# Kernel tuning notes

Hardware: AMD Instinct MI355X
Metric: run time of the kernel (lower is better)

## Reference

```python
import jax, jax.numpy as jnp
import numpy as np


def gcn_conv(x, edge_index, W, b):
    """PyG-style GCNConv: add self loops, symmetric normalization, sum-aggregate."""
    N = x.shape[0]
    loop = jnp.arange(N, dtype=edge_index.dtype)
    src = jnp.concatenate([edge_index[0], loop])
    dst = jnp.concatenate([edge_index[1], loop])
    # degree computed on target (col) index with unit edge weights
    deg = jax.ops.segment_sum(jnp.ones_like(dst, dtype=x.dtype), dst, num_segments=N)
    dinv = jnp.where(deg > 0, jax.lax.rsqrt(deg), 0.0)
    norm = dinv[src] * dinv[dst]            # [E+N]
    h = x @ W                               # [N, out]
    msg = h[src] * norm[:, None]            # gather + scale
    out = jax.ops.segment_sum(msg, dst, num_segments=N)  # scatter-add
    return out + b


def global_mean_pool(x, batch, num_graphs):
    s = jax.ops.segment_sum(x, batch, num_segments=num_graphs)
    cnt = jax.ops.segment_sum(jnp.ones((x.shape[0],), x.dtype), batch, num_segments=num_graphs)
    return s / jnp.maximum(cnt, 1.0)[:, None]


NUM_GRAPHS = 64


def setup_inputs() -> dict:
    key = jax.random.key(0)
    ks = jax.random.split(key, 20)
    N, E = 100000, 1600000
    inp = {
        "x_origin": jax.random.normal(ks[0], (N, 25), jnp.float32),
        "edge_index_origin": jax.random.randint(ks[1], (2, E), 0, N, jnp.int64),
        "batch_origin": jnp.sort(jax.random.randint(ks[2], (N,), 0, NUM_GRAPHS, jnp.int64)),
        "x_line": jax.random.normal(ks[3], (N, 51), jnp.float32),
        "edge_index_line": jax.random.randint(ks[4], (2, E), 0, N, jnp.int64),
        "batch_line": jnp.sort(jax.random.randint(ks[5], (N,), 0, NUM_GRAPHS, jnp.int64)),
        # learned params (Glorot-ish scale)
        "W1": jax.random.normal(ks[6], (25, 128), jnp.float32) * 0.1,
        "b1": jnp.zeros((128,), jnp.float32),
        "W2": jax.random.normal(ks[7], (128, 64), jnp.float32) * 0.08,
        "b2": jnp.zeros((64,), jnp.float32),
        "W5": jax.random.normal(ks[8], (64, 5), jnp.float32) * 0.1,
        "b5": jnp.zeros((5,), jnp.float32),
        "W3": jax.random.normal(ks[9], (51, 64), jnp.float32) * 0.1,
        "b3": jnp.zeros((64,), jnp.float32),
        "W4": jax.random.normal(ks[10], (64, 5), jnp.float32) * 0.1,
        "b4": jnp.zeros((5,), jnp.float32),
        "Wfc": jax.random.normal(ks[11], (10, 2), jnp.float32) * 0.2,
        "bfc": jnp.zeros((2,), jnp.float32),
    }
    return inp


def reference(x_origin, edge_index_origin, batch_origin,
              x_line, edge_index_line, batch_line,
              W1, b1, W2, b2, W5, b5, W3, b3, W4, b4, Wfc, bfc):
    # origin branch
    h = jax.nn.relu(gcn_conv(x_origin, edge_index_origin, W1, b1))
    h = jax.nn.relu(gcn_conv(h, edge_index_origin, W2, b2))
    h = gcn_conv(h, edge_index_origin, W5, b5)
    g_origin = global_mean_pool(h, batch_origin, NUM_GRAPHS)  # [G, 5]
    # line branch
    hl = jax.nn.relu(gcn_conv(x_line, edge_index_line, W3, b3))
    hl = gcn_conv(hl, edge_index_line, W4, b4)
    g_line = global_mean_pool(hl, batch_line, NUM_GRAPHS)     # [G, 5]
    x = jnp.concatenate([g_origin, g_line], axis=1) @ Wfc + bfc  # [G, 2]
    return jax.nn.log_softmax(x, axis=1)
```

## Files before the change

### kernel.cpp

```cpp
#include <hip/hip_runtime.h>
#include <math.h>

#define NUM_G 64
#define CAP 32
#define SL 128
#define CHUNK_Q 1024
#define SEGCAP 32
#define MAXR 800
#define MAXNBA 1024
#define LSTR 33
#define ABLK 512

typedef unsigned short u16;
typedef unsigned int u32;
typedef int vint4 __attribute__((ext_vector_type(4)));
typedef short bf16x8 __attribute__((ext_vector_type(8)));
typedef float f32x4 __attribute__((ext_vector_type(4)));

__device__ inline u16 f2bf(float f) {
    u32 u = __float_as_uint(f);
    u32 r = u + 0x7FFF + ((u >> 16) & 1);
    return (u16)(r >> 16);
}
__device__ inline float bf2f(u16 h) { return __uint_as_float((u32)h << 16); }
__device__ inline float bflo(u32 p) { return __uint_as_float(p << 16); }
__device__ inline float bfhi(u32 p) { return __uint_as_float(p & 0xFFFF0000u); }

__device__ inline int slice_of(int d, float pinv) {
    int s = (int)((float)d * pinv);
    return s > SL - 1 ? SL - 1 : s;
}


__global__ void k_bin(const int* __restrict__ ei_o, const int* __restrict__ ei_l,
                      u32* __restrict__ binbuf, int* __restrict__ cntbuf,
                      int E, int NBA, float pinv) {
    __shared__ int lcnt[2 * SL];
    for (int i = threadIdx.x; i < 2 * SL; i += 256) lcnt[i] = 0;
    __syncthreads();
    const int qE = E >> 2;
    const int TQ = 2 * qE;
    const int b = blockIdx.x;
    for (int k = 0; k < CHUNK_Q; k += 256) {
        int qi = b * CHUNK_Q + k + threadIdx.x;
        if (qi >= TQ) break;
        int g = qi >= qE;
        int e4 = (g ? qi - qE : qi) * 4;
        const int* ei = g ? ei_l : ei_o;
        vint4 d4 = __builtin_nontemporal_load((const vint4*)(ei + E + e4));
        vint4 s4 = __builtin_nontemporal_load((const vint4*)(ei + e4));
        #pragma unroll
        for (int j = 0; j < 4; j++) {
            int d = d4[j];
            int bin = g * SL + slice_of(d, pinv);
            int rank = atomicAdd(&lcnt[bin], 1);
            if (rank < SEGCAP) {
                u32 pk = ((u32)(d & 1023) << 17) | (u32)s4[j];
                binbuf[((size_t)(bin * NBA + b)) * SEGCAP + rank] = pk;
            }
        }
    }
    __syncthreads();
    for (int i = threadIdx.x; i < 2 * SL; i += 256)
        cntbuf[i * NBA + b] = min(lcnt[i], SEGCAP);
}

__global__ __launch_bounds__(ABLK, 1)
void k_assemble(const u32* __restrict__ binbuf, const int* __restrict__ cntbuf,
                const int* __restrict__ ei_o, const int* __restrict__ ei_l,
                int* __restrict__ adj_o, int* __restrict__ adj_l,
                int* __restrict__ deg_o, int* __restrict__ deg_l,
                float* __restrict__ dinv_o, float* __restrict__ dinv_l,
                const float* __restrict__ x_o, const float* __restrict__ x_l,
                u16* __restrict__ Xpo, u16* __restrict__ Xpl,
                int N, int E, int NBA, float pinv) {
    const int g = blockIdx.x >> 7;
    const int s = blockIdx.x & (SL - 1);

    int lo, hi;
    { int a = 0, b2 = N; while (a < b2) { int m = (a + b2) >> 1;
        if (slice_of(m, pinv) >= s) b2 = m; else a = m + 1; } lo = a; }
    { int a = lo, b2 = N; while (a < b2) { int m = (a + b2) >> 1;
        if (slice_of(m, pinv) >= s + 1) b2 = m; else a = m + 1; } hi = a; }
    const int R = hi - lo;

    __shared__ int ladj[MAXR * LSTR];
    __shared__ int cnt[MAXR];
    __shared__ int segcnt[MAXNBA];
    __shared__ float sdinv[MAXR];
    for (int i = threadIdx.x; i < R; i += ABLK) cnt[i] = 0;
    const int bin = g * SL + s;
    for (int i = threadIdx.x; i < NBA; i += ABLK) segcnt[i] = cntbuf[bin * NBA + i];
    __syncthreads();

    const u32* base = binbuf + (size_t)bin * NBA * SEGCAP;
    const int total = NBA * SEGCAP;
    const int lo10 = lo & 1023;
    for (int i = threadIdx.x; i < total; i += ABLK) {
        int seg = i >> 5;
        int idx = i & (SEGCAP - 1);
        if (idx >= segcnt[seg]) continue;
        u32 pk = __builtin_nontemporal_load(base + i);
        int drel = ((int)(pk >> 17) - lo10) & 1023;
        int src = (int)(pk & 0x1FFFFu);
        int r = atomicAdd(&cnt[drel], 1);
        if (r < CAP) ladj[drel * LSTR + r] = src;
    }
    int tbase = (E >> 2) * 4, rem = E - tbase;
    if (threadIdx.x < rem) {
        const int* ei = g ? ei_l : ei_o;
        int e = tbase + threadIdx.x;
        int d = ei[E + e];
        if (d >= lo && d < hi) {
            int r = atomicAdd(&cnt[d - lo], 1);
            if (r < CAP) ladj[(d - lo) * LSTR + r] = ei[e];
        }
    }
    __syncthreads();

    for (int r = threadIdx.x; r < R; r += ABLK) {
        int c = min(cnt[r], CAP);
        int* row = &ladj[r * LSTR];
        int v[CAP];
        #pragma unroll
        for (int a = 0; a < CAP; a++) v[a] = (a < c) ? row[a] : 0x7FFFFFFF;
        #pragma unroll
        for (int k = 2; k <= CAP; k <<= 1) {
            #pragma unroll
            for (int j = k >> 1; j > 0; j >>= 1) {
                #pragma unroll
                for (int i = 0; i < CAP; i++) {
                    int ixj = i ^ j;
                    if (ixj > i) {
                        bool up = ((i & k) == 0);
                        int a = v[i], b = v[ixj];
                        bool sw = up ? (a > b) : (a < b);
                        v[i] = sw ? b : a;
                        v[ixj] = sw ? a : b;
                    }
                }
            }
        }
        #pragma unroll
        for (int a = 0; a < CAP; a++) row[a] = v[a];
    }
    __syncthreads();

    int* adj = g ? adj_l : adj_o;
    int* deg = g ? deg_l : deg_o;
    float* dinv = g ? dinv_l : dinv_o;
    for (int i = threadIdx.x; i < R * CAP; i += ABLK) {
        int r = i >> 5, c = i & 31;
        adj[(size_t)lo * CAP + i] = ladj[r * LSTR + c];
    }
    for (int i = threadIdx.x; i < R; i += ABLK) {
        int c = cnt[i];
        deg[lo + i] = c;
        float dv = rsqrtf((float)(c + 1));
        dinv[lo + i] = dv;
        sdinv[i] = dv;
    }
    __syncthreads();

    const float* xsrc = g ? x_l : x_o;
    u16* Xp = g ? Xpl : Xpo;
    const int FR = g ? 51 : 25;
    const int SH = g ? 6 : 5;
    const int FC = 1 << SH;
    for (int i = threadIdx.x; i < (R << SH); i += ABLK) {
        int r = i >> SH, c = i & (FC - 1);
        float val = (c < FR) ? xsrc[(size_t)(lo + r) * FR + c] * sdinv[r] : 0.f;
        Xp[((size_t)(lo + r) << SH) + c] = f2bf(val);
    }
}


template <int K, int F, int MODE>
__device__ void gemm_body(u16* Wt, int bidx, const u16* __restrict__ X,
                          const float* __restrict__ W, const float* __restrict__ sb,
                          u16* __restrict__ S, int N, int Kreal) {
    const int KP = K + 8;
    for (int i = threadIdx.x; i < Kreal * F; i += 256) {
        int k = i / F, n = i % F;
        Wt[n * KP + k] = f2bf(W[i]);
    }
    for (int i = threadIdx.x; i < (K - Kreal) * F; i += 256) {
        int k = Kreal + i / F, n = i % F;
        Wt[n * KP + k] = 0;
    }
    __syncthreads();

    const int wave = threadIdx.x >> 6;
    const int lane = threadIdx.x & 63;
    const int m = lane & 15;
    const int kgrp = lane >> 4;
    const int row0 = bidx * 64 + wave * 16;
    const int arow = row0 + m;
    const bool ok = arow < N;

    bf16x8 afrag[K / 32];
    const u16* xr = X + (size_t)arow * K;
    #pragma unroll
    for (int kc = 0; kc < K / 32; kc++) {
        if (ok) afrag[kc] = *(const bf16x8*)(xr + kc * 32 + kgrp * 8);
        else    afrag[kc] = bf16x8{0, 0, 0, 0, 0, 0, 0, 0};
    }

    #pragma unroll
    for (int nt = 0; nt < F / 16; nt++) {
        f32x4 acc = f32x4{0.f, 0.f, 0.f, 0.f};
        #pragma unroll
        for (int kc = 0; kc < K / 32; kc++) {
            bf16x8 bfrag = *(const bf16x8*)(&Wt[(nt * 16 + m) * KP + kc * 32 + kgrp * 8]);
            acc = __builtin_amdgcn_mfma_f32_16x16x32_bf16(afrag[kc], bfrag, acc, 0, 0, 0);
        }
        #pragma unroll
        for (int r = 0; r < 4; r++) {
            int orow = row0 + kgrp * 4 + r;
            if (orow < N) {
                float o;
                if (MODE == 0) o = acc[r] * sb[orow];
                else { o = acc[r] + sb[nt * 16 + m]; o = fmaxf(o, 0.f); }
                S[(size_t)orow * F + nt * 16 + m] = f2bf(o);
            }
        }
    }
}

__device__ void small_body(float* Ws, int bidx, const u16* __restrict__ X,
                           const float* __restrict__ W, const float* __restrict__ dinv,
                           float* __restrict__ S, int N, int K, int F) {
    int KF = K * F;
    for (int i = threadIdx.x; i < KF; i += 256) Ws[i] = W[i];
    __syncthreads();
    int idx = bidx * 256 + threadIdx.x;
    if (idx >= N * F) return;
    int row = idx / F;
    int col = idx - row * F;
    const uint4* xq = (const uint4*)(X + (size_t)row * K);
    float acc = 0.f;
    for (int k8 = 0; k8 < K / 8; k8++) {
        uint4 p = xq[k8];
        const float* wk = Ws + (k8 * 8) * F + col;
        acc = fmaf(bflo(p.x), wk[0 * F], acc);
        acc = fmaf(bfhi(p.x), wk[1 * F], acc);
        acc = fmaf(bflo(p.y), wk[2 * F], acc);
        acc = fmaf(bfhi(p.y), wk[3 * F], acc);
        acc = fmaf(bflo(p.z), wk[4 * F], acc);
        acc = fmaf(bfhi(p.z), wk[5 * F], acc);
        acc = fmaf(bflo(p.w), wk[6 * F], acc);
        acc = fmaf(bfhi(p.w), wk[7 * F], acc);
    }
    S[idx] = acc * dinv[row];
}

__device__ void agg8_body(int bidx, const u16* __restrict__ S, const int* __restrict__ deg,
                          const int* __restrict__ adj, const float* __restrict__ dinv,
                          const float* __restrict__ bias, u16* __restrict__ Y,
                          int N, int F8, int relu) {
    int idx = bidx * 256 + threadIdx.x;
    if (idx >= N * F8) return;
    int v = idx / F8;
    int f8 = idx - v * F8;
    const uint4* Sq = (const uint4*)S;

    uint4 p = Sq[(size_t)v * F8 + f8];
    float a0 = bflo(p.x), a1 = bfhi(p.x), a2 = bflo(p.y), a3 = bfhi(p.y);
    float a4 = bflo(p.z), a5 = bfhi(p.z), a6 = bflo(p.w), a7 = bfhi(p.w);

    int dg = min(deg[v], CAP);
    const int* av = adj + v * CAP;
    int i = 0;
    for (; i + 4 <= dg; i += 4) {
        vint4 u4 = *(const vint4*)(av + i);
        uint4 q0 = Sq[(size_t)u4.x * F8 + f8];
        uint4 q1 = Sq[(size_t)u4.y * F8 + f8];
        uint4 q2 = Sq[(size_t)u4.z * F8 + f8];
        uint4 q3 = Sq[(size_t)u4.w * F8 + f8];
        a0 += bflo(q0.x); a1 += bfhi(q0.x); a2 += bflo(q0.y); a3 += bfhi(q0.y);
        a4 += bflo(q0.z); a5 += bfhi(q0.z); a6 += bflo(q0.w); a7 += bfhi(q0.w);
        a0 += bflo(q1.x); a1 += bfhi(q1.x); a2 += bflo(q1.y); a3 += bfhi(q1.y);
        a4 += bflo(q1.z); a5 += bfhi(q1.z); a6 += bflo(q1.w); a7 += bfhi(q1.w);
        a0 += bflo(q2.x); a1 += bfhi(q2.x); a2 += bflo(q2.y); a3 += bfhi(q2.y);
        a4 += bflo(q2.z); a5 += bfhi(q2.z); a6 += bflo(q2.w); a7 += bfhi(q2.w);
        a0 += bflo(q3.x); a1 += bfhi(q3.x); a2 += bflo(q3.y); a3 += bfhi(q3.y);
        a4 += bflo(q3.z); a5 += bfhi(q3.z); a6 += bflo(q3.w); a7 += bfhi(q3.w);
    }
    for (; i < dg; i++) {
        int u = av[i];
        uint4 q = Sq[(size_t)u * F8 + f8];
        a0 += bflo(q.x); a1 += bfhi(q.x);
        a2 += bflo(q.y); a3 += bfhi(q.y);
        a4 += bflo(q.z); a5 += bfhi(q.z);
        a6 += bflo(q.w); a7 += bfhi(q.w);
    }
    float dv = dinv[v];
    const float* bp = bias + 8 * f8;
    float o[8] = {dv*a0 + bp[0], dv*a1 + bp[1], dv*a2 + bp[2], dv*a3 + bp[3],
                  dv*a4 + bp[4], dv*a5 + bp[5], dv*a6 + bp[6], dv*a7 + bp[7]};
    if (relu) {
        #pragma unroll
        for (int j = 0; j < 8; j++) o[j] = fmaxf(o[j], 0.f);
    }
    uint4 pk;
    pk.x = (u32)f2bf(o[0]) | ((u32)f2bf(o[1]) << 16);
    pk.y = (u32)f2bf(o[2]) | ((u32)f2bf(o[3]) << 16);
    pk.z = (u32)f2bf(o[4]) | ((u32)f2bf(o[5]) << 16);
    pk.w = (u32)f2bf(o[6]) | ((u32)f2bf(o[7]) << 16);
    *(uint4*)(Y + (size_t)v * (F8 * 8) + f8 * 8) = pk;
}

__device__ void agg5_pool_body(int bidx, const float* __restrict__ S, const int* __restrict__ deg,
                               const int* __restrict__ adj, const float* __restrict__ dinv,
                               const float* __restrict__ bias, const int* __restrict__ batch,
                               float* __restrict__ gsum, float* __restrict__ gcnt, int N) {
    __shared__ float sacc[NUM_G * 5];
    __shared__ float scnt[NUM_G];
    for (int i = threadIdx.x; i < NUM_G * 5; i += 256) sacc[i] = 0.f;
    for (int i = threadIdx.x; i < NUM_G; i += 256) scnt[i] = 0.f;
    __syncthreads();
    int v = bidx * 256 + threadIdx.x;
    if (v < N) {
        const float* sv = S + v * 5;
        float a0 = sv[0], a1 = sv[1], a2 = sv[2], a3 = sv[3], a4 = sv[4];
        int dg = min(deg[v], CAP);
        const int* av = adj + v * CAP;
        int i = 0;
        for (; i + 2 <= dg; i += 2) {
            int ua = av[i], ub = av[i + 1];
            const float* pa = S + ua * 5;
            const float* pb = S + ub * 5;
            float b0 = pa[0], b1 = pa[1], b2 = pa[2], b3 = pa[3], b4 = pa[4];
            float c0 = pb[0], c1 = pb[1], c2 = pb[2], c3 = pb[3], c4 = pb[4];
            a0 += b0 + c0; a1 += b1 + c1; a2 += b2 + c2; a3 += b3 + c3; a4 += b4 + c4;
        }
        for (; i < dg; i++) {
            const float* p = S + av[i] * 5;
            a0 += p[0]; a1 += p[1]; a2 += p[2]; a3 += p[3]; a4 += p[4];
        }
        float dv = dinv[v];
        int b = batch[v];
        atomicAdd(&sacc[b * 5 + 0], dv * a0 + bias[0]);
        atomicAdd(&sacc[b * 5 + 1], dv * a1 + bias[1]);
        atomicAdd(&sacc[b * 5 + 2], dv * a2 + bias[2]);
        atomicAdd(&sacc[b * 5 + 3], dv * a3 + bias[3]);
        atomicAdd(&sacc[b * 5 + 4], dv * a4 + bias[4]);
        atomicAdd(&scnt[b], 1.f);
    }
    __syncthreads();
    for (int i = threadIdx.x; i < NUM_G * 5; i += 256)
        if (sacc[i] != 0.f) atomicAdd(&gsum[i], sacc[i]);
    for (int i = threadIdx.x; i < NUM_G; i += 256)
        if (scnt[i] != 0.f) atomicAdd(&gcnt[i], scnt[i]);
}


__global__ __launch_bounds__(256)
void k_preagg_both(const u16* Xpo, const int* deg_o, const int* adj_o,
                   const float* dinv_o, const float* zb, u16* Ao,
                   const u16* Xpl, const int* deg_l, const int* adj_l,
                   const float* dinv_l, u16* Al, int N, int nbA) {
    if ((int)blockIdx.x < nbA)
        agg8_body(blockIdx.x, Xpo, deg_o, adj_o, dinv_o, zb, Ao, N, 4, 0);
    else
        agg8_body(blockIdx.x - nbA, Xpl, deg_l, adj_l, dinv_l, zb, Al, N, 8, 0);
}

__global__ __launch_bounds__(256)
void k_gemm1_both(const u16* Ao, const float* W1, const float* b1, u16* H1,
                  const u16* Al, const float* W3, const float* b3, u16* HL1,
                  int N, int nbA) {
    __shared__ u16 Wt[5120];
    if ((int)blockIdx.x < nbA)
        gemm_body<32, 128, 1>(Wt, blockIdx.x, Ao, W1, b1, H1, N, 25);
    else
        gemm_body<64, 64, 1>(Wt, blockIdx.x - nbA, Al, W3, b3, HL1, N, 51);
}

__global__ __launch_bounds__(256)
void k_gemm2_both(const u16* H1, const float* W2, const float* dinv_o, u16* S2,
                  const u16* HL1, const float* W4, const float* dinv_l, float* S5l,
                  int N, int nbA) {
    __shared__ float smem[4352];
    if ((int)blockIdx.x < nbA)
        gemm_body<128, 64, 0>((u16*)smem, blockIdx.x, H1, W2, dinv_o, S2, N, 128);
    else
        small_body(smem, blockIdx.x - nbA, HL1, W4, dinv_l, S5l, N, 64, 5);
}

__global__ __launch_bounds__(256)
void k_aggpool_both(const u16* S2, const int* deg_o, const int* adj_o,
                    const float* dinv_o, const float* b2, u16* H2,
                    const float* S5l, const int* deg_l, const int* adj_l,
                    const float* dinv_l, const float* b4, const int* bat_l,
                    float* gsum_l, float* gcnt_l, int N, int nbA) {
    if ((int)blockIdx.x < nbA)
        agg8_body(blockIdx.x, S2, deg_o, adj_o, dinv_o, b2, H2, N, 8, 1);
    else
        agg5_pool_body(blockIdx.x - nbA, S5l, deg_l, adj_l, dinv_l, b4, bat_l,
                       gsum_l, gcnt_l, N);
}

__global__ __launch_bounds__(256)
void k_gemm_small(const u16* X, const float* W, const float* dinv,
                  float* S, int N, int K, int F) {
    __shared__ float Ws[512];
    small_body(Ws, blockIdx.x, X, W, dinv, S, N, K, F);
}

__global__ __launch_bounds__(256)
void k_agg5_pool(const float* S, const int* deg, const int* adj, const float* dinv,
                 const float* bias, const int* batch,
                 float* gsum, float* gcnt, int N) {
    agg5_pool_body(blockIdx.x, S, deg, adj, dinv, bias, batch, gsum, gcnt, N);
}

__global__ void k_head(const float* __restrict__ gsum_o, const float* __restrict__ gcnt_o,
                       const float* __restrict__ gsum_l, const float* __restrict__ gcnt_l,
                       const float* __restrict__ Wfc, const float* __restrict__ bfc,
                       float* __restrict__ out, int G) {
    int g = threadIdx.x;
    if (g >= G) return;
    float feat[10];
    float co = fmaxf(gcnt_o[g], 1.f);
    float cl = fmaxf(gcnt_l[g], 1.f);
    for (int f = 0; f < 5; f++) feat[f]     = gsum_o[g * 5 + f] / co;
    for (int f = 0; f < 5; f++) feat[5 + f] = gsum_l[g * 5 + f] / cl;
    float z0 = bfc[0], z1 = bfc[1];
    for (int i = 0; i < 10; i++) {
        z0 += feat[i] * Wfc[i * 2 + 0];
        z1 += feat[i] * Wfc[i * 2 + 1];
    }
    float m = fmaxf(z0, z1);
    float lse = m + logf(expf(z0 - m) + expf(z1 - m));
    out[g * 2 + 0] = z0 - lse;
    out[g * 2 + 1] = z1 - lse;
}


extern "C" void kernel_launch(void* const* d_in, const int* in_sizes, int n_in,
                              void* d_out, int out_size, void* d_ws, size_t ws_size,
                              hipStream_t stream) {
    const float* x_o   = (const float*)d_in[0];
    const int*   ei_o  = (const int*)d_in[1];
    const int*   bat_o = (const int*)d_in[2];
    const float* x_l   = (const float*)d_in[3];
    const int*   ei_l  = (const int*)d_in[4];
    const int*   bat_l = (const int*)d_in[5];
    const float* W1  = (const float*)d_in[6];   const float* b1  = (const float*)d_in[7];
    const float* W2  = (const float*)d_in[8];   const float* b2  = (const float*)d_in[9];
    const float* W5  = (const float*)d_in[10];  const float* b5  = (const float*)d_in[11];
    const float* W3  = (const float*)d_in[12];  const float* b3  = (const float*)d_in[13];
    const float* W4  = (const float*)d_in[14];  const float* b4  = (const float*)d_in[15];
    const float* Wfc = (const float*)d_in[16];  const float* bfc = (const float*)d_in[17];
    float* out = (float*)d_out;

    const int N = in_sizes[0] / 25;
    const int E = in_sizes[1] / 2;
    const int G = NUM_G;

    int nb = (N + 255) / 256;
    int nb64 = (N + 63) / 64;
    int TQ = 2 * (E >> 2);
    int NBA = (TQ + CHUNK_Q - 1) / CHUNK_Q;

    float* gsum_o = (float*)d_ws;
    float* gsum_l = gsum_o + G * 5;
    float* gcnt_o = gsum_l + G * 5;
    float* gcnt_l = gcnt_o + G;
    float* zb     = gcnt_l + G;
    int* deg_o = (int*)(zb + 64);
    int* deg_l = deg_o + N;
    float* dinv_o = (float*)(deg_l + N);
    float* dinv_l = dinv_o + N;
    int* cntbuf = (int*)(dinv_l + N);
    int* adj_o = cntbuf + 2 * SL * NBA;
    int* adj_l = adj_o + (size_t)N * CAP;
    u16* bufA = (u16*)(adj_l + (size_t)N * CAP);
    u16* bufB = bufA + (size_t)N * 128;
    u16* Xpo  = bufB + (size_t)N * 128;
    u16* Xpl  = Xpo + (size_t)N * 32;

    u32* binbuf = (u32*)bufA;
    u16* Ao  = bufB;
    u16* Al  = bufB + (size_t)N * 32;
    u16* H1  = bufA;
    u16* HL1 = Xpl;
    u16* S2  = bufB;
    float* S5l = (float*)(bufB + (size_t)N * 64);
    u16* H2  = bufA;
    float* S5o = (float*)Xpo;

    size_t zero_bytes = (size_t)(2 * G * 5 + 2 * G + 64) * sizeof(float);
    hipMemsetAsync(d_ws, 0, zero_bytes, stream);

    float pinv = (float)SL / (float)N;
    k_bin<<<NBA, 256, 0, stream>>>(ei_o, ei_l, binbuf, cntbuf, E, NBA, pinv);
    k_assemble<<<2 * SL, ABLK, 0, stream>>>(binbuf, cntbuf, ei_o, ei_l,
                                            adj_o, adj_l, deg_o, deg_l,
                                            dinv_o, dinv_l, x_o, x_l, Xpo, Xpl,
                                            N, E, NBA, pinv);

    int nb_pA = (N * 4 + 255) / 256;
    int nb_pB = (N * 8 + 255) / 256;
    k_preagg_both<<<nb_pA + nb_pB, 256, 0, stream>>>(Xpo, deg_o, adj_o, dinv_o, zb, Ao,
                                                     Xpl, deg_l, adj_l, dinv_l, Al,
                                                     N, nb_pA);
    k_gemm1_both<<<2 * nb64, 256, 0, stream>>>(Ao, W1, b1, H1, Al, W3, b3, HL1, N, nb64);
    int nb_sL = (N * 5 + 255) / 256;
    k_gemm2_both<<<nb64 + nb_sL, 256, 0, stream>>>(H1, W2, dinv_o, S2,
                                                   HL1, W4, dinv_l, S5l, N, nb64);
    int nb_a = (N * 8 + 255) / 256;
    k_aggpool_both<<<nb_a + nb, 256, 0, stream>>>(S2, deg_o, adj_o, dinv_o, b2, H2,
                                                  S5l, deg_l, adj_l, dinv_l, b4, bat_l,
                                                  gsum_l, gcnt_l, N, nb_a);
    k_gemm_small<<<nb_sL, 256, 0, stream>>>(H2, W5, dinv_o, S5o, N, 64, 5);
    k_agg5_pool<<<nb, 256, 0, stream>>>(S5o, deg_o, adj_o, dinv_o, b5, bat_o,
                                        gsum_o, gcnt_o, N);
    k_head<<<1, 64, 0, stream>>>(gsum_o, gcnt_o, gsum_l, gcnt_l, Wfc, bfc, out, G);
}
```

Measured before the change: 401.2 us.

## Split assemble slices into halves and move feature prep to separate kernel

Each adjacency-assembly block now handles half a node slice, which doubles the grid to 512 blocks and roughly halves shared-memory use per block. Launch bounds change to allow four blocks per CU, improving occupancy on a kernel that previously ran about one 512-thread block per CU. The per-node feature scaling and bf16 packing moves into a new fully parallel k_prep kernel. The cost is that each half-block rereads and filters the whole bin's packed edges, so binbuf reads double, and there is one extra launch plus a round trip of dinv through global memory.

Result: faster. 367.6 us (-8.4%).

```diff
diff --git a/kernel.cpp b/kernel.cpp
--- a/kernel.cpp
+++ b/kernel.cpp
@@ -6,8 +6,8 @@
 #define SL 128
 #define CHUNK_Q 1024
 #define SEGCAP 32
-#define MAXR 800
-#define MAXNBA 1024
+#define MAXR2 400
+#define MAXNBA 800
 #define LSTR 33
 #define ABLK 512
 
@@ -65,43 +65,46 @@
         cntbuf[i * NBA + b] = min(lcnt[i], SEGCAP);
 }
 
-__global__ __launch_bounds__(ABLK, 1)
+__global__ __launch_bounds__(ABLK, 4)
 void k_assemble(const u32* __restrict__ binbuf, const int* __restrict__ cntbuf,
                 const int* __restrict__ ei_o, const int* __restrict__ ei_l,
                 int* __restrict__ adj_o, int* __restrict__ adj_l,
                 int* __restrict__ deg_o, int* __restrict__ deg_l,
                 float* __restrict__ dinv_o, float* __restrict__ dinv_l,
-                const float* __restrict__ x_o, const float* __restrict__ x_l,
-                u16* __restrict__ Xpo, u16* __restrict__ Xpl,
                 int N, int E, int NBA, float pinv) {
-    const int g = blockIdx.x >> 7;
-    const int s = blockIdx.x & (SL - 1);
+    const int g = blockIdx.x >> 8;
+    const int sh = blockIdx.x & 255;
+    const int s = sh >> 1;
+    const int half = sh & 1;
 
     int lo, hi;
     { int a = 0, b2 = N; while (a < b2) { int m = (a + b2) >> 1;
         if (slice_of(m, pinv) >= s) b2 = m; else a = m + 1; } lo = a; }
     { int a = lo, b2 = N; while (a < b2) { int m = (a + b2) >> 1;
         if (slice_of(m, pinv) >= s + 1) b2 = m; else a = m + 1; } hi = a; }
-    const int R = hi - lo;
-
-    __shared__ int ladj[MAXR * LSTR];
-    __shared__ int cnt[MAXR];
+    const int mid = lo + ((hi - lo + 1) >> 1);
+    const int lo2 = half ? mid : lo;
+    const int hi2 = half ? hi : mid;
+    const int R2 = hi2 - lo2;
+
+    __shared__ int ladj[MAXR2 * LSTR];
+    __shared__ int cnt[MAXR2];
     __shared__ int segcnt[MAXNBA];
-    __shared__ float sdinv[MAXR];
-    for (int i = threadIdx.x; i < R; i += ABLK) cnt[i] = 0;
+    for (int i = threadIdx.x; i < R2; i += ABLK) cnt[i] = 0;
     const int bin = g * SL + s;
     for (int i = threadIdx.x; i < NBA; i += ABLK) segcnt[i] = cntbuf[bin * NBA + i];
     __syncthreads();
 
     const u32* base = binbuf + (size_t)bin * NBA * SEGCAP;
     const int total = NBA * SEGCAP;
-    const int lo10 = lo & 1023;
+    const int lo10 = lo2 & 1023;
     for (int i = threadIdx.x; i < total; i += ABLK) {
         int seg = i >> 5;
         int idx = i & (SEGCAP - 1);
         if (idx >= segcnt[seg]) continue;
         u32 pk = __builtin_nontemporal_load(base + i);
         int drel = ((int)(pk >> 17) - lo10) & 1023;
+        if (drel >= R2) continue;
         int src = (int)(pk & 0x1FFFFu);
         int r = atomicAdd(&cnt[drel], 1);
         if (r < CAP) ladj[drel * LSTR + r] = src;
@@ -111,14 +114,14 @@
         const int* ei = g ? ei_l : ei_o;
         int e = tbase + threadIdx.x;
         int d = ei[E + e];
-        if (d >= lo && d < hi) {
-            int r = atomicAdd(&cnt[d - lo], 1);
-            if (r < CAP) ladj[(d - lo) * LSTR + r] = ei[e];
-        }
-    }
-    __syncthreads();
-
-    for (int r = threadIdx.x; r < R; r += ABLK) {
+        if (d >= lo2 && d < hi2) {
+            int r = atomicAdd(&cnt[d - lo2], 1);
+            if (r < CAP) ladj[(d - lo2) * LSTR + r] = ei[e];
+        }
+    }
+    __syncthreads();
+
+    for (int r = threadIdx.x; r < R2; r += ABLK) {
         int c = min(cnt[r], CAP);
         int* row = &ladj[r * LSTR];
         int v[CAP];
@@ -149,28 +152,33 @@
     int* adj = g ? adj_l : adj_o;
     int* deg = g ? deg_l : deg_o;
     float* dinv = g ? dinv_l : dinv_o;
-    for (int i = threadIdx.x; i < R * CAP; i += ABLK) {
+    for (int i = threadIdx.x; i < R2 * CAP; i += ABLK) {
         int r = i >> 5, c = i & 31;
-        adj[(size_t)lo * CAP + i] = ladj[r * LSTR + c];
-    }
-    for (int i = threadIdx.x; i < R; i += ABLK) {
+        adj[(size_t)lo2 * CAP + i] = ladj[r * LSTR + c];
+    }
+    for (int i = threadIdx.x; i < R2; i += ABLK) {
         int c = cnt[i];
-        deg[lo + i] = c;
-        float dv = rsqrtf((float)(c + 1));
-        dinv[lo + i] = dv;
-        sdinv[i] = dv;
-    }
-    __syncthreads();
-
-    const float* xsrc = g ? x_l : x_o;
-    u16* Xp = g ? Xpl : Xpo;
-    const int FR = g ? 51 : 25;
-    const int SH = g ? 6 : 5;
-    const int FC = 1 << SH;
-    for (int i = threadIdx.x; i < (R << SH); i += ABLK) {
-        int r = i >> SH, c = i & (FC - 1);
-        float val = (c < FR) ? xsrc[(size_t)(lo + r) * FR + c] * sdinv[r] : 0.f;
-        Xp[((size_t)(lo + r) << SH) + c] = f2bf(val);
+        deg[lo2 + i] = c;
+        dinv[lo2 + i] = rsqrtf((float)(c + 1));
+    }
+}
+
+__global__ void k_prep(const float* __restrict__ xo, const float* __restrict__ xl,
+                       const float* __restrict__ dinv_o, const float* __restrict__ dinv_l,
+                       u16* __restrict__ Xpo, u16* __restrict__ Xpl, int N) {
+    int idx = blockIdx.x * 256 + threadIdx.x;
+    int t1 = N * 32;
+    if (idx < t1) {
+        int v = idx >> 5, c = idx & 31;
+        float val = (c < 25) ? xo[(size_t)v * 25 + c] * dinv_o[v] : 0.f;
+        Xpo[idx] = f2bf(val);
+    } else {
+        int j = idx - t1;
+        if (j < N * 64) {
+            int v = j >> 6, c = j & 63;
+            float val = (c < 51) ? xl[(size_t)v * 51 + c] * dinv_l[v] : 0.f;
+            Xpl[j] = f2bf(val);
+        }
     }
 }
 
@@ -496,10 +504,10 @@
 
     float pinv = (float)SL / (float)N;
     k_bin<<<NBA, 256, 0, stream>>>(ei_o, ei_l, binbuf, cntbuf, E, NBA, pinv);
-    k_assemble<<<2 * SL, ABLK, 0, stream>>>(binbuf, cntbuf, ei_o, ei_l,
+    k_assemble<<<4 * SL, ABLK, 0, stream>>>(binbuf, cntbuf, ei_o, ei_l,
                                             adj_o, adj_l, deg_o, deg_l,
-                                            dinv_o, dinv_l, x_o, x_l, Xpo, Xpl,
-                                            N, E, NBA, pinv);
+                                            dinv_o, dinv_l, N, E, NBA, pinv);
+    k_prep<<<(N * 96 + 255) / 256, 256, 0, stream>>>(x_o, x_l, dinv_o, dinv_l, Xpo, Xpl, N);
 
     int nb_pA = (N * 4 + 255) / 256;
     int nb_pB = (N * 8 + 255) / 256;
```
